# Kernel optimization log

Measured on AMD Instinct MI355X. Metric: run time of the kernel, lower is better.

## Reference

```python
import jax, jax.numpy as jnp
import numpy as np

NEG = -1.0e9  # padding value so max(row) > 0.5 is False for non-existent neighbors


def _mlp_score(x, W1, b1, W2, b2, W3, b3):
    # consistency MLP: 8 -> 32 -> 16 -> 1, sigmoid
    h = jax.nn.relu(x @ W1 + b1)
    h = jax.nn.relu(h @ W2 + b2)
    return jax.nn.sigmoid(h @ W3 + b3)[..., 0]  # [B, S]


def _nearby_any(flags, window):
    # flags: [B, S] bool; returns True where any flag within +/-window
    B, S = flags.shape
    p = jnp.pad(flags, ((0, 0), (window, window)))
    shifted = jnp.stack([p[:, k:k + S] for k in range(2 * window + 1)], axis=0)
    return jnp.any(shifted, axis=0)


def _forward(aspect_logits, opinion_logits, rel, explicit_aspects, explicit_opinions,
             W1, b1, W2, b2, W3, b3):
    B, S, _ = aspect_logits.shape

    # --- rule 1: consistency penalty (applies to whole row) ---
    combined = jnp.concatenate([aspect_logits, opinion_logits], axis=-1)  # [B,S,8]
    score = _mlp_score(combined, W1, b1, W2, b2, W3, b3)                  # [B,S]
    # if score < 0.5: row *= 1 - (0.5 - score)*2 == 2*score
    factor1 = jnp.where(score < 0.5, 2.0 * score, 1.0)[..., None]         # [B,S,1]

    # --- rule 2/3: implicit prob > 0.5 and no nearby explicit element ---
    pa = jax.nn.softmax(aspect_logits, axis=-1)[..., :2].sum(-1) > 0.5
    po = jax.nn.softmax(opinion_logits, axis=-1)[..., :2].sum(-1) > 0.5
    near_op = _nearby_any(explicit_opinions > 0, window=3)
    near_as = _nearby_any(explicit_aspects > 0, window=3)
    r2 = pa & jnp.logical_not(near_op)   # aspect[:2] *= 0.3
    r3 = po & jnp.logical_not(near_as)   # opinion[:2] *= 0.3

    # --- rule 4: causality ordering (depends only on original relations) ---
    m = rel > 0.5                               # [B,S,S,R]
    strength = jnp.any(m, axis=(-1, -2))        # [B,S]  (max > 0.5)
    related = jnp.any(m, axis=-1)               # [B,S,S]: for row i, flags over positions j
    idx = jnp.arange(S)
    before = idx[None, :] < idx[:, None]        # [i, j]: j < i
    r4 = strength & jnp.any(related & before[None], axis=-1)  # aspect[:2] *= 0.7

    fa2 = jnp.where(r2, 0.3, 1.0) * jnp.where(r4, 0.7, 1.0)   # [B,S]
    fo2 = jnp.where(r3, 0.3, 1.0)

    a_base = aspect_logits * factor1
    a_base = jnp.concatenate([a_base[..., :2] * fa2[..., None], a_base[..., 2:]], axis=-1)
    o_base = opinion_logits * factor1
    o_base = jnp.concatenate([o_base[..., :2] * fo2[..., None], o_base[..., 2:]], axis=-1)

    # --- isolation rule: sequential along seq (prev neighbors are already-final,
    #     next neighbors are the ORIGINAL logits, self is excluded) ---
    a_pad = jnp.concatenate([aspect_logits, jnp.full((B, 2, 4), NEG, aspect_logits.dtype)], axis=1)
    o_pad = jnp.concatenate([opinion_logits, jnp.full((B, 2, 4), NEG, opinion_logits.dtype)], axis=1)

    xs = (
        jnp.swapaxes(a_base, 0, 1),           # [S,B,4]
        jnp.swapaxes(o_base, 0, 1),
        jnp.swapaxes(a_pad[:, 1:S + 1], 0, 1),  # next1 (original)
        jnp.swapaxes(a_pad[:, 2:S + 2], 0, 1),  # next2
        jnp.swapaxes(o_pad[:, 1:S + 1], 0, 1),
        jnp.swapaxes(o_pad[:, 2:S + 2], 0, 1),
    )

    neg_row = jnp.full((B, 4), NEG, aspect_logits.dtype)
    carry0 = (neg_row, neg_row, neg_row, neg_row)  # a_prev2, a_prev1, o_prev2, o_prev1

    def act(row):
        return row.max(axis=-1) > 0.5

    def step(carry, x):
        ap2, ap1, op2, op1 = carry
        a_b, o_b, an1, an2, on1, on2 = x
        activity = (act(ap2) | act(ap1) | act(op2) | act(op1)
                    | act(an1) | act(an2) | act(on1) | act(on2))  # [B]
        f = jnp.where(activity, 1.0, 0.1)[:, None]
        a_fin = jnp.concatenate([a_b[:, :2] * f, a_b[:, 2:]], axis=1)
        o_fin = jnp.concatenate([o_b[:, :2] * f, o_b[:, 2:]], axis=1)
        return (ap1, a_fin, op1, o_fin), (a_fin, o_fin)

    _, (a_out, o_out) = jax.lax.scan(step, carry0, xs)
    return jnp.swapaxes(a_out, 0, 1), jnp.swapaxes(o_out, 0, 1)


def setup_inputs() -> dict:
    key = jax.random.key(0)
    ks = jax.random.split(key, 12)
    B, S, R = 8, 512, 8
    inp = {
        "aspect_logits": jax.random.normal(ks[0], (B, S, 4), jnp.float32),
        "opinion_logits": jax.random.normal(ks[1], (B, S, 4), jnp.float32),
        "aspect_opinion_relations": jax.random.uniform(ks[2], (B, S, S, R), jnp.float32),
        "explicit_aspects": jax.random.randint(ks[3], (B, S), 0, 2, jnp.int32),
        "explicit_opinions": jax.random.randint(ks[4], (B, S), 0, 2, jnp.int32),
        "W1": jax.random.normal(ks[5], (8, 32), jnp.float32) * 0.3,
        "b1": jnp.zeros((32,), jnp.float32),
        "W2": jax.random.normal(ks[6], (32, 16), jnp.float32) * 0.2,
        "b2": jnp.zeros((16,), jnp.float32),
        "W3": jax.random.normal(ks[7], (16, 1), jnp.float32) * 0.2,
        "b3": jnp.zeros((1,), jnp.float32),
    }
    return inp


def reference(aspect_logits, opinion_logits, aspect_opinion_relations,
              explicit_aspects, explicit_opinions, W1, b1, W2, b2, W3, b3):
    return _forward(aspect_logits, opinion_logits, aspect_opinion_relations,
                    explicit_aspects, explicit_opinions, W1, b1, W2, b2, W3, b3)
```

## Files before the change

### kernel.cpp

```cpp
#include <hip/hip_runtime.h>


#define B 8
#define S 512
#define NROWS (B * S)
#define NTH 256


__global__ __launch_bounds__(NTH) void iqe_main(
    const float* __restrict__ aL, const float* __restrict__ oL,
    const float* __restrict__ rel,
    const int* __restrict__ exA, const int* __restrict__ exO,
    const float* __restrict__ W1, const float* __restrict__ b1,
    const float* __restrict__ W2, const float* __restrict__ b2,
    const float* __restrict__ W3, const float* __restrict__ b3,
    float* __restrict__ out, unsigned char* __restrict__ flags)
{
    const int wave = ((blockIdx.x * NTH) + threadIdx.x) >> 6;
    const int lane = threadIdx.x & 63;
    const int s = wave & (S - 1);
    const int b = wave >> 9;

    const float* relrow = rel + (size_t)wave * (S * 8);
    const int jloc = lane >> 3;
    float relv0 = 0.0f;
    if (s > 0 && jloc < s) relv0 = relrow[lane];

    const float4 av4 = ((const float4*)aL)[wave];
    const float4 ov4 = ((const float4*)oL)[wave];
    float x[8] = {av4.x, av4.y, av4.z, av4.w, ov4.x, ov4.y, ov4.z, ov4.w};

    const int lo = (s - 3 < 0) ? 0 : s - 3;
    const int hi = (s + 3 > S - 1) ? S - 1 : s + 3;
    const int win = hi - lo + 1;
    bool myOp = false, myAs = false;
    if (lane < win) {
        const int k = b * S + lo + lane;
        myOp = exO[k] > 0;
        myAs = exA[k] > 0;
    }
    const bool nearOp = __any(myOp);
    const bool nearAs = __any(myAs);

    const float amax = fmaxf(fmaxf(x[0], x[1]), fmaxf(x[2], x[3]));
    const float omax = fmaxf(fmaxf(x[4], x[5]), fmaxf(x[6], x[7]));
    const float ea0 = expf(x[0] - amax), ea1 = expf(x[1] - amax);
    const float ea2 = expf(x[2] - amax), ea3 = expf(x[3] - amax);
    const float eo0 = expf(x[4] - omax), eo1 = expf(x[5] - omax);
    const float eo2 = expf(x[6] - omax), eo3 = expf(x[7] - omax);
    const bool pa = (ea0 + ea1) > (ea2 + ea3);
    const bool po = (eo0 + eo1) > (eo2 + eo3);

    const int u = lane & 31;
    float h1 = b1[u];
#pragma unroll
    for (int k = 0; k < 8; ++k) h1 = fmaf(x[k], W1[k * 32 + u], h1);
    h1 = fmaxf(h1, 0.0f);

    const int v16 = lane & 15;
    float h2 = b2[v16];
#pragma unroll
    for (int uu = 0; uu < 32; ++uu) {
        float hu = __shfl(h1, uu, 64);
        h2 = fmaf(hu, W2[uu * 16 + v16], h2);
    }
    h2 = fmaxf(h2, 0.0f);

    float part = h2 * W3[v16];
    part += __shfl_xor(part, 8, 16);
    part += __shfl_xor(part, 4, 16);
    part += __shfl_xor(part, 2, 16);
    part += __shfl_xor(part, 1, 16);
    const float z = part + b3[0];
    const float score = 1.0f / (1.0f + expf(-z));
    const float factor1 = (z < 0.0f) ? 2.0f * score : 1.0f;

    bool r4 = __any(relv0 > 0.5f);
    for (int j0 = 8; j0 < s && !r4; j0 += 8) {
        float v = (j0 + jloc < s) ? relrow[j0 * 8 + lane] : 0.0f;
        r4 = __any(v > 0.5f);
    }

    const bool r2 = pa && !nearOp;
    const bool r3 = po && !nearAs;
    const float fa2 = (r2 ? 0.3f : 1.0f) * (r4 ? 0.7f : 1.0f);
    const float fo2 = (r3 ? 0.3f : 1.0f);

    const float ab0 = (x[0] * factor1) * fa2;
    const float ab1 = (x[1] * factor1) * fa2;
    const float ab2 = x[2] * factor1;
    const float ab3 = x[3] * factor1;
    const float ob0 = (x[4] * factor1) * fo2;
    const float ob1 = (x[5] * factor1) * fo2;
    const float ob2 = x[6] * factor1;
    const float ob3 = x[7] * factor1;

    const float m1 = fmaxf(fmaxf(fmaxf(ab0, ab1), fmaxf(ab2, ab3)),
                           fmaxf(fmaxf(ob0, ob1), fmaxf(ob2, ob3)));
    const float m0 = fmaxf(fmaxf(fmaxf(ab0 * 0.1f, ab1 * 0.1f), fmaxf(ab2, ab3)),
                           fmaxf(fmaxf(ob0 * 0.1f, ob1 * 0.1f), fmaxf(ob2, ob3)));
    const bool h1bit = m1 > 0.5f;
    const bool h0bit = m0 > 0.5f;
    const bool orig = (amax > 0.5f) || (omax > 0.5f);

    if (lane == 0) {
        float4* outa = (float4*)out;
        float4* outo = (float4*)(out + NROWS * 4);
        outa[wave] = make_float4(ab0, ab1, ab2, ab3);
        outo[wave] = make_float4(ob0, ob1, ob2, ob3);
        flags[wave] = (unsigned char)((h1bit ? 1 : 0) | (h0bit ? 2 : 0) | (orig ? 4 : 0));
    }
}

__global__ __launch_bounds__(512) void iqe_scan(
    const unsigned char* __restrict__ flags, float* __restrict__ out)
{
    __shared__ unsigned char sflags[NROWS];
    __shared__ unsigned char sf[NROWS];
    const int tid = threadIdx.x;

    for (int i = tid; i < NROWS; i += 512) sflags[i] = flags[i];
    __syncthreads();

    if (tid < B) {
        const unsigned char* fb = sflags + tid * S;
        unsigned char* fo = sf + tid * S;
        bool hp1 = false, hp2 = false;
#pragma unroll 4
        for (int s = 0; s < S; ++s) {
            bool n = false;
            if (s + 1 < S) n |= (fb[s + 1] & 4) != 0;
            if (s + 2 < S) n |= (fb[s + 2] & 4) != 0;
            const bool activity = hp1 | hp2 | n;
            const unsigned char fl = fb[s];
            const bool h = activity ? ((fl & 1) != 0) : ((fl & 2) != 0);
            fo[s] = activity ? 1 : 0;
            hp2 = hp1; hp1 = h;
        }
    }
    __syncthreads();

    for (int row = tid; row < NROWS; row += 512) {
        if (!sf[row]) {
            float2* pa = (float2*)(out + (size_t)row * 4);
            float2* po = (float2*)(out + (size_t)(NROWS + row) * 4);
            float2 a = *pa, o = *po;
            a.x *= 0.1f; a.y *= 0.1f;
            o.x *= 0.1f; o.y *= 0.1f;
            *pa = a; *po = o;
        }
    }
}

extern "C" void kernel_launch(void* const* d_in, const int* in_sizes, int n_in,
                              void* d_out, int out_size, void* d_ws, size_t ws_size,
                              hipStream_t stream) {
    const float* aL  = (const float*)d_in[0];
    const float* oL  = (const float*)d_in[1];
    const float* rel = (const float*)d_in[2];
    const int*   exA = (const int*)d_in[3];
    const int*   exO = (const int*)d_in[4];
    const float* W1  = (const float*)d_in[5];
    const float* b1  = (const float*)d_in[6];
    const float* W2  = (const float*)d_in[7];
    const float* b2  = (const float*)d_in[8];
    const float* W3  = (const float*)d_in[9];
    const float* b3  = (const float*)d_in[10];

    float* out = (float*)d_out;
    unsigned char* flags = (unsigned char*)d_ws;

    const int nblocks = NROWS / (NTH / 64);
    iqe_main<<<nblocks, NTH, 0, stream>>>(aL, oL, rel, exA, exO,
                                          W1, b1, W2, b2, W3, b3, out, flags);
    iqe_scan<<<1, 512, 0, stream>>>(flags, out);
}
```

Before: 154.1 us.

## Rewrite causal scan with bit-packed masks and sparse inactive-row fixup

The single-block scan kernel now packs the per-row flag bytes into 64-bit bitmasks with a multiply trick. It computes the look-ahead neighbour mask with shifts and runs the serial recurrence on register bitmasks instead of byte loads from shared memory. The fixup pass walks only the set bits of the inactive mask, using 64 threads instead of striding 512 threads over all rows. This aims to shorten the latency-bound serial scan. The trade-off is that the fixup becomes serialized per thread when many rows are inactive.

```diff
diff --git a/kernel.cpp b/kernel.cpp
--- a/kernel.cpp
+++ b/kernel.cpp
@@ -5,6 +5,8 @@
 #define S 512
 #define NROWS (B * S)
 #define NTH 256
+
+typedef unsigned long long u64;
 
 
 __global__ __launch_bounds__(NTH) void iqe_main(
@@ -112,43 +114,69 @@
     }
 }
 
-__global__ __launch_bounds__(512) void iqe_scan(
+__device__ __forceinline__ u64 pack8(u64 x) {
+    return (x * 0x0102040810204080ULL) >> 56;
+}
+
+__global__ __launch_bounds__(64) void iqe_scan2(
     const unsigned char* __restrict__ flags, float* __restrict__ out)
 {
-    __shared__ unsigned char sflags[NROWS];
-    __shared__ unsigned char sf[NROWS];
-    const int tid = threadIdx.x;
-
-    for (int i = tid; i < NROWS; i += 512) sflags[i] = flags[i];
+    __shared__ u64 sh1[64], sh0[64], snm[64], sact[64];
+    const int t = threadIdx.x;
+    const int b = t >> 3;
+    const int w = t & 7;
+
+    const u64* fp = (const u64*)(flags + (size_t)b * S + (size_t)w * 64);
+    u64 h1m = 0, h0m = 0, orm = 0;
+#pragma unroll
+    for (int c = 0; c < 8; ++c) {
+        const u64 v = fp[c];
+        h1m |= pack8(v        & 0x0101010101010101ULL) << (8 * c);
+        h0m |= pack8((v >> 1) & 0x0101010101010101ULL) << (8 * c);
+        orm |= pack8((v >> 2) & 0x0101010101010101ULL) << (8 * c);
+    }
+
+    u64 ornext = __shfl(orm, (t + 1) & 63, 64);
+    if (w == 7) ornext = 0;
+    const u64 nm = (orm >> 1) | (ornext << 63) | (orm >> 2) | (ornext << 62);
+
+    sh1[t] = h1m; sh0[t] = h0m; snm[t] = nm;
     __syncthreads();
 
-    if (tid < B) {
-        const unsigned char* fb = sflags + tid * S;
-        unsigned char* fo = sf + tid * S;
-        bool hp1 = false, hp2 = false;
-#pragma unroll 4
-        for (int s = 0; s < S; ++s) {
-            bool n = false;
-            if (s + 1 < S) n |= (fb[s + 1] & 4) != 0;
-            if (s + 2 < S) n |= (fb[s + 2] & 4) != 0;
-            const bool activity = hp1 | hp2 | n;
-            const unsigned char fl = fb[s];
-            const bool h = activity ? ((fl & 1) != 0) : ((fl & 2) != 0);
-            fo[s] = activity ? 1 : 0;
-            hp2 = hp1; hp1 = h;
+    if (t < B) {
+        const int base = t * 8;
+        unsigned int hp1 = 0, hp2 = 0;
+        for (int ww = 0; ww < 8; ++ww) {
+            u64 h1w = sh1[base + ww];
+            u64 h0w = sh0[base + ww];
+            u64 nw  = snm[base + ww];
+            u64 aw  = 0;
+            for (int i = 0; i < 64; ++i) {
+                const unsigned int act = hp1 | hp2 | (unsigned int)(nw & 1u);
+                const unsigned int h =
+                    (unsigned int)((act ? h1w : h0w) & 1u);
+                aw |= (u64)act << i;
+                hp2 = hp1; hp1 = h;
+                h1w >>= 1; h0w >>= 1; nw >>= 1;
+            }
+            sact[base + ww] = aw;
         }
     }
     __syncthreads();
 
-    for (int row = tid; row < NROWS; row += 512) {
-        if (!sf[row]) {
-            float2* pa = (float2*)(out + (size_t)row * 4);
-            float2* po = (float2*)(out + (size_t)(NROWS + row) * 4);
-            float2 a = *pa, o = *po;
-            a.x *= 0.1f; a.y *= 0.1f;
-            o.x *= 0.1f; o.y *= 0.1f;
-            *pa = a; *po = o;
-        }
+    const u64 aw = sact[t];
+    u64 inact = ~aw;
+    const int row0 = b * S + w * 64;
+    while (inact) {
+        const int i = __builtin_ctzll(inact);
+        inact &= inact - 1;
+        const int row = row0 + i;
+        float2* pa = (float2*)(out + (size_t)row * 4);
+        float2* po = (float2*)(out + (size_t)(NROWS + row) * 4);
+        float2 a = *pa, o = *po;
+        a.x *= 0.1f; a.y *= 0.1f;
+        o.x *= 0.1f; o.y *= 0.1f;
+        *pa = a; *po = o;
     }
 }
 
@@ -173,5 +201,5 @@
     const int nblocks = NROWS / (NTH / 64);
     iqe_main<<<nblocks, NTH, 0, stream>>>(aL, oL, rel, exA, exO,
                                           W1, b1, W2, b2, W3, b3, out, flags);
-    iqe_scan<<<1, 512, 0, stream>>>(flags, out);
-}
+    iqe_scan2<<<1, 64, 0, stream>>>(flags, out);
+}
```

Result: faster. 124.5 us (-19.2%).
